# Optimization experiments

Hardware: AMD Instinct MI355X
Metric: run time of the kernel (lower is better)

## Reference

```python
import jax, jax.numpy as jnp
import numpy as np

N = 100000      # nodes
E = 1600000     # edges (before self-loops)
F_IN = 128      # num_features
H = 4           # heads
C = 32          # out_channels per head (num_hidden)
SLOPE = 0.2     # leaky relu negative slope (alpha)


def setup_inputs() -> dict:
    key = jax.random.key(0)
    k = jax.random.split(key, 6)
    x = jax.random.normal(k[0], (N, F_IN), jnp.float32)
    edge_index = jax.random.randint(k[1], (2, E), 0, N, dtype=jnp.int64)
    W = jax.random.normal(k[2], (F_IN, H * C), jnp.float32) * (1.0 / np.sqrt(F_IN))
    att_src = jax.random.normal(k[3], (H, C), jnp.float32) * 0.1
    att_dst = jax.random.normal(k[4], (H, C), jnp.float32) * 0.1
    bias = jnp.zeros((H * C,), jnp.float32)
    return dict(x=x, W=W, att_src=att_src, att_dst=att_dst, bias=bias,
                edge_index=edge_index)


def reference(x, W, att_src, att_dst, bias, edge_index):
    # PyG GATConv (concat=True, add_self_loops=True), eval mode (dropout off).
    loops = jnp.arange(N, dtype=edge_index.dtype)
    ei = jnp.concatenate([edge_index, jnp.stack([loops, loops])], axis=1)
    src, dst = ei[0], ei[1]                     # [E+N]

    h = (x @ W).reshape(N, H, C)                # projected node features
    a_src = jnp.einsum('nhc,hc->nh', h, att_src)   # [N, H]
    a_dst = jnp.einsum('nhc,hc->nh', h, att_dst)   # [N, H]

    e = a_src[src] + a_dst[dst]                 # [E+N, H]
    e = jnp.where(e > 0, e, SLOPE * e)          # leaky relu

    # segment softmax over incoming edges of each dst node (per head)
    m = jax.lax.stop_gradient(jax.ops.segment_max(e, dst, num_segments=N))
    p = jnp.exp(e - m[dst])
    denom = jax.ops.segment_sum(p, dst, num_segments=N)
    alpha = p / (denom[dst] + 1e-16)            # [E+N, H]

    # weighted scatter-aggregate of source features
    out = jax.ops.segment_sum(alpha[:, :, None] * h[src], dst, num_segments=N)
    return out.reshape(N, H * C) + bias
```

## Files before the change

### kernel.cpp

```cpp
#include <hip/hip_runtime.h>
#include <hip/hip_bf16.h>
#include <math.h>

#define N_NODES 100000
#define F_IN    128
#define HC      128
#define NH      4
#define SLOPE   0.2f

#define NB      196
#define BSH     9
#define CAP     10240
#define CHUNK   8192
#define PADK    136

typedef __attribute__((ext_vector_type(8))) short short8;
typedef __attribute__((ext_vector_type(4))) float f32x4;
typedef __attribute__((ext_vector_type(2))) float fx2;

static __device__ __forceinline__ float leaky(float x) { return x > 0.f ? x : SLOPE * x; }

static __device__ __forceinline__ short f2bs(float f) {
    __hip_bfloat16 b = __float2bfloat16(f);
    return *reinterpret_cast<short*>(&b);
}

__global__ __launch_bounds__(256) void k_gemm(const float* __restrict__ x,
                                              const float* __restrict__ W,
                                              const float* __restrict__ att_src,
                                              const float* __restrict__ att_dst,
                                              unsigned short* __restrict__ hb,
                                              float* __restrict__ a_src,
                                              float* __restrict__ a_dst)
{
    __shared__ short xs[64 * PADK];
    __shared__ short ws[128 * PADK];
    const int t  = threadIdx.x;
    const int r0 = blockIdx.x * 64;

    for (int i = t; i < 2048; i += 256) {
        int row = i >> 5, kq = (i & 31) * 4;
        int gr = r0 + row;
        float4 v = make_float4(0.f, 0.f, 0.f, 0.f);
        if (gr < N_NODES) v = ((const float4*)(x + (size_t)gr * F_IN))[i & 31];
        short* p = &xs[row * PADK + kq];
        p[0] = f2bs(v.x); p[1] = f2bs(v.y); p[2] = f2bs(v.z); p[3] = f2bs(v.w);
    }
    for (int i = t; i < 4096; i += 256) {
        int k = i >> 5, nq = (i & 31) * 4;
        float4 v = *(const float4*)&W[k * HC + nq];
        ws[(nq + 0) * PADK + k] = f2bs(v.x);
        ws[(nq + 1) * PADK + k] = f2bs(v.y);
        ws[(nq + 2) * PADK + k] = f2bs(v.z);
        ws[(nq + 3) * PADK + k] = f2bs(v.w);
    }
    __syncthreads();

    const int wave = t >> 6, lane = t & 63;
    const int quad = lane >> 4, l16 = lane & 15;
    const int wrow = wave * 16;

    f32x4 acc[8];
    #pragma unroll
    for (int nt = 0; nt < 8; ++nt) acc[nt] = (f32x4){0.f, 0.f, 0.f, 0.f};

    const short* ap = &xs[(wrow + l16) * PADK + quad * 8];
    #pragma unroll
    for (int kb = 0; kb < 4; ++kb) {
        short8 a = *(const short8*)(ap + kb * 32);
        #pragma unroll
        for (int nt = 0; nt < 8; ++nt) {
            short8 b = *(const short8*)&ws[(nt * 16 + l16) * PADK + kb * 32 + quad * 8];
            acc[nt] = __builtin_amdgcn_mfma_f32_16x16x32_bf16(a, b, acc[nt], 0, 0, 0);
        }
    }

    float att_s[8], att_d[8];
    #pragma unroll
    for (int nt = 0; nt < 8; ++nt) {
        att_s[nt] = att_src[nt * 16 + l16];
        att_d[nt] = att_dst[nt * 16 + l16];
    }

    #pragma unroll
    for (int g = 0; g < 4; ++g) {
        int r = r0 + wrow + quad * 4 + g;
        if (r < N_NODES) {
            #pragma unroll
            for (int nt = 0; nt < 8; ++nt)
                hb[(size_t)r * HC + nt * 16 + l16] = (unsigned short)f2bs(acc[nt][g]);
        }
        float s0 = acc[0][g] * att_s[0] + acc[1][g] * att_s[1];
        float s1 = acc[2][g] * att_s[2] + acc[3][g] * att_s[3];
        float s2 = acc[4][g] * att_s[4] + acc[5][g] * att_s[5];
        float s3 = acc[6][g] * att_s[6] + acc[7][g] * att_s[7];
        float d0 = acc[0][g] * att_d[0] + acc[1][g] * att_d[1];
        float d1 = acc[2][g] * att_d[2] + acc[3][g] * att_d[3];
        float d2 = acc[4][g] * att_d[4] + acc[5][g] * att_d[5];
        float d3 = acc[6][g] * att_d[6] + acc[7][g] * att_d[7];
        #pragma unroll
        for (int o = 1; o < 16; o <<= 1) {
            s0 += __shfl_xor(s0, o); s1 += __shfl_xor(s1, o);
            s2 += __shfl_xor(s2, o); s3 += __shfl_xor(s3, o);
            d0 += __shfl_xor(d0, o); d1 += __shfl_xor(d1, o);
            d2 += __shfl_xor(d2, o); d3 += __shfl_xor(d3, o);
        }
        if (l16 == 0 && r < N_NODES) {
            *(float4*)&a_src[r * NH] = make_float4(s0, s1, s2, s3);
            *(float4*)&a_dst[r * NH] = make_float4(d0, d1, d2, d3);
        }
    }
}

__global__ __launch_bounds__(256) void k_bucket(const int* __restrict__ srcp,
                                                const int* __restrict__ dstp,
                                                int* __restrict__ bucket_cursor,
                                                int* __restrict__ eb, int E)
{
    __shared__ int ebuf[CHUNK];
    __shared__ unsigned char bkt[CHUNK];
    __shared__ int hist[256];
    __shared__ int lexcl[257];
    __shared__ int gbase[256];
    __shared__ int sdata[256];

    const int t = threadIdx.x;
    const int base = blockIdx.x * CHUNK;

    hist[t] = 0;
    __syncthreads();

    #pragma unroll
    for (int j = 0; j < CHUNK / 256; ++j) {
        int i = base + t + j * 256;
        if (i < E) atomicAdd(&hist[dstp[i] >> BSH], 1);
    }
    __syncthreads();

    int cnt = hist[t];
    sdata[t] = cnt;
    __syncthreads();
    for (int o = 1; o < 256; o <<= 1) {
        int add = (t >= o) ? sdata[t - o] : 0;
        __syncthreads();
        sdata[t] += add;
        __syncthreads();
    }
    int excl = sdata[t] - cnt;
    lexcl[t] = excl;
    if (t == 255) lexcl[256] = sdata[255];
    hist[t] = excl;
    int gb = 0;
    if (t < NB && cnt > 0) gb = atomicAdd(&bucket_cursor[t], cnt);
    gbase[t] = t * CAP + gb;
    __syncthreads();

    #pragma unroll
    for (int j = 0; j < CHUNK / 256; ++j) {
        int i = base + t + j * 256;
        if (i < E) {
            int s = srcp[i], d = dstp[i];
            int b = d >> BSH;
            int r = atomicAdd(&hist[b], 1);
            ebuf[r] = (s << BSH) | (d & 511);
            bkt[r] = (unsigned char)b;
        }
    }
    __syncthreads();

    const int blockTotal = lexcl[256];
    for (int i = t; i < blockTotal; i += 256) {
        int b = bkt[i];
        eb[gbase[b] + (i - lexcl[b])] = ebuf[i];
    }
}

__global__ void k_bscan(const int* __restrict__ bucket_cursor,
                        int* __restrict__ bexcl)
{
    __shared__ int sdata[256];
    const int t = threadIdx.x;
    int nvalid = 0;
    if (t < NB) {
        int n0 = t * 512;
        nvalid = min(512, N_NODES - n0);
        if (nvalid < 0) nvalid = 0;
    }
    int v = (t < NB) ? bucket_cursor[t] + nvalid : 0;
    sdata[t] = v;
    __syncthreads();
    for (int o = 1; o < 256; o <<= 1) {
        int add = (t >= o) ? sdata[t - o] : 0;
        __syncthreads();
        sdata[t] += add;
        __syncthreads();
    }
    if (t < NB) bexcl[t] = sdata[t] - v;
}

__global__ __launch_bounds__(256) void k_csr(const int* __restrict__ eb,
                                             const int* __restrict__ bucket_cursor,
                                             const int* __restrict__ bexcl,
                                             int* __restrict__ col,
                                             int2* __restrict__ rowse)
{
    __shared__ int deg[512];
    __shared__ int sdata[256];

    const int t  = threadIdx.x;
    const int b  = blockIdx.x;
    const int n0 = b * 512;
    const int cnt   = bucket_cursor[b];
    const int ebase = b * CAP;
    const int gofs  = bexcl[b];

    deg[t]       = (n0 + t       < N_NODES) ? 1 : 0;
    deg[t + 256] = (n0 + t + 256 < N_NODES) ? 1 : 0;
    __syncthreads();

    for (int i = t; i < cnt; i += 256)
        atomicAdd(&deg[eb[ebase + i] & 511], 1);
    __syncthreads();

    int d0 = deg[2 * t], d1 = deg[2 * t + 1];
    int ps = d0 + d1;
    sdata[t] = ps;
    __syncthreads();
    for (int o = 1; o < 256; o <<= 1) {
        int add = (t >= o) ? sdata[t - o] : 0;
        __syncthreads();
        sdata[t] += add;
        __syncthreads();
    }
    int e0 = sdata[t] - ps;
    int e1 = e0 + d0;
    __syncthreads();

    int na = n0 + 2 * t, nb2 = n0 + 2 * t + 1;
    if (na < N_NODES) {
        rowse[na] = make_int2(gofs + e0, gofs + e0 + d0);
        col[gofs + e0] = na;
    }
    if (nb2 < N_NODES) {
        rowse[nb2] = make_int2(gofs + e1, gofs + e1 + d1);
        col[gofs + e1] = nb2;
    }
    deg[2 * t]     = e0 + 1;
    deg[2 * t + 1] = e1 + 1;
    __syncthreads();

    for (int i = t; i < cnt; i += 256) {
        int v = eb[ebase + i];
        int r = atomicAdd(&deg[v & 511], 1);
        col[gofs + r] = v >> BSH;
    }
}

__global__ __launch_bounds__(256) void k_node(const unsigned short* __restrict__ hb,
                                              const float* __restrict__ a_src,
                                              const float* __restrict__ a_dst,
                                              const int2* __restrict__ rowse,
                                              const int* __restrict__ col,
                                              const float* __restrict__ bias,
                                              float* __restrict__ out)
{
    const int lane = threadIdx.x & 63;
    const int node = blockIdx.x * 4 + (threadIdx.x >> 6);
    if (node >= N_NODES) return;

    const int2 se = rowse[node];
    const int r0 = se.x, r1 = se.y;
    const int myh = lane >> 4;
    const float adm = a_dst[node * NH + myh];

    float denom = 0.f, acc0 = 0.f, acc1 = 0.f;
    int i = r0;
    for (; i + 8 <= r1; i += 8) {
        int s[8];
        #pragma unroll
        for (int j = 0; j < 8; ++j) s[j] = col[i + j];
        float as[8];
        #pragma unroll
        for (int j = 0; j < 8; ++j) as[j] = a_src[s[j] * NH + myh];
        unsigned int hv[8];
        #pragma unroll
        for (int j = 0; j < 8; ++j)
            hv[j] = *(const unsigned int*)&hb[(size_t)s[j] * HC + 2 * lane];
        #pragma unroll
        for (int j = 0; j < 8; ++j) {
            float p = __expf(leaky(as[j] + adm));
            denom += p;
            acc0 += p * __uint_as_float(hv[j] << 16);
            acc1 += p * __uint_as_float(hv[j] & 0xffff0000u);
        }
    }
    for (; i < r1; ++i) {
        int s = col[i];
        float p = __expf(leaky(a_src[s * NH + myh] + adm));
        unsigned int v = *(const unsigned int*)&hb[(size_t)s * HC + 2 * lane];
        denom += p;
        acc0 += p * __uint_as_float(v << 16);
        acc1 += p * __uint_as_float(v & 0xffff0000u);
    }

    float inv = 1.f / (denom + 1e-16f);
    fx2 o2;
    o2.x = acc0 * inv + bias[2 * lane];
    o2.y = acc1 * inv + bias[2 * lane + 1];
    __builtin_nontemporal_store(o2, (fx2*)&out[(size_t)node * HC + 2 * lane]);
}

extern "C" void kernel_launch(void* const* d_in, const int* in_sizes, int n_in,
                              void* d_out, int out_size, void* d_ws, size_t ws_size,
                              hipStream_t stream)
{
    const float* x       = (const float*)d_in[0];
    const float* W       = (const float*)d_in[1];
    const float* att_src = (const float*)d_in[2];
    const float* att_dst = (const float*)d_in[3];
    const float* bias    = (const float*)d_in[4];
    const int*   ei      = (const int*)d_in[5];
    const int E = in_sizes[5] / 2;
    const int* srcp = ei;
    const int* dstp = ei + E;
    float* out = (float*)d_out;

    char* wsb = (char*)d_ws;
    size_t off = 0;
    auto alloc = [&](size_t bytes) -> char* {
        char* p = wsb + off;
        off += (bytes + 255) & ~(size_t)255;
        return p;
    };
    unsigned short* hb = (unsigned short*)alloc((size_t)N_NODES * HC * sizeof(unsigned short));
    float* a_src   = (float*)alloc((size_t)N_NODES * NH * sizeof(float));
    float* a_dst   = (float*)alloc((size_t)N_NODES * NH * sizeof(float));
    int*   eb      = (int*)alloc((size_t)NB * CAP * sizeof(int));
    int*   col     = (int*)alloc((size_t)(E + N_NODES) * sizeof(int));
    int2*  rowse   = (int2*)alloc((size_t)N_NODES * sizeof(int2));
    int*   bcursor = (int*)alloc(256 * sizeof(int));
    int*   bexcl   = (int*)alloc(256 * sizeof(int));

    (void)hipMemsetAsync(bcursor, 0, 256 * sizeof(int), stream);

    k_gemm<<<(N_NODES + 63) / 64, 256, 0, stream>>>(x, W, att_src, att_dst,
                                                    hb, a_src, a_dst);
    k_bucket<<<(E + CHUNK - 1) / CHUNK, 256, 0, stream>>>(srcp, dstp, bcursor, eb, E);
    k_bscan<<<1, 256, 0, stream>>>(bcursor, bexcl);
    k_csr<<<NB, 256, 0, stream>>>(eb, bcursor, bexcl, col, rowse);
    k_node<<<(N_NODES + 3) / 4, 256, 0, stream>>>(hb, a_src, a_dst, rowse, col, bias, out);
}
```

Baseline: 291.6 us.

## Pre-transpose W once, pad bucket cursors, shrink bucket chunks, widen CSR blocks

Adds a small prep kernel that converts W to bf16 and transposes it once, so each GEMM block copies it with vector loads instead of redoing the strided conversion. Bucket cursors are padded so per-bucket atomics land on separate cache lines. The bucket chunk size drops, giving more blocks for the scatter phase. The CSR build runs 1024 threads per block to use more of the GPU across its 196 blocks. These trade an extra launch and more global atomics for better parallelism and less redundant work.

New measurement: 265.8 us. -8.8%, faster.

```diff
diff --git a/kernel.cpp b/kernel.cpp
--- a/kernel.cpp
+++ b/kernel.cpp
@@ -8,11 +8,13 @@
 #define NH      4
 #define SLOPE   0.2f
 
+#define PADK    136
+
 #define NB      196
 #define BSH     9
 #define CAP     10240
-#define CHUNK   8192
-#define PADK    136
+#define CHUNK   2048
+#define CURPAD  16
 
 typedef __attribute__((ext_vector_type(8))) short short8;
 typedef __attribute__((ext_vector_type(4))) float f32x4;
@@ -25,8 +27,18 @@
     return *reinterpret_cast<short*>(&b);
 }
 
+__global__ __launch_bounds__(256) void k_prep(const float* __restrict__ W,
+                                              unsigned short* __restrict__ wt)
+{
+    int t = blockIdx.x * 256 + threadIdx.x;
+    if (t < 128 * 128) {
+        int k = t >> 7, n = t & 127;
+        wt[n * 128 + k] = (unsigned short)f2bs(W[k * HC + n]);
+    }
+}
+
 __global__ __launch_bounds__(256) void k_gemm(const float* __restrict__ x,
-                                              const float* __restrict__ W,
+                                              const unsigned short* __restrict__ wt,
                                               const float* __restrict__ att_src,
                                               const float* __restrict__ att_dst,
                                               unsigned short* __restrict__ hb,
@@ -46,13 +58,9 @@
         short* p = &xs[row * PADK + kq];
         p[0] = f2bs(v.x); p[1] = f2bs(v.y); p[2] = f2bs(v.z); p[3] = f2bs(v.w);
     }
-    for (int i = t; i < 4096; i += 256) {
-        int k = i >> 5, nq = (i & 31) * 4;
-        float4 v = *(const float4*)&W[k * HC + nq];
-        ws[(nq + 0) * PADK + k] = f2bs(v.x);
-        ws[(nq + 1) * PADK + k] = f2bs(v.y);
-        ws[(nq + 2) * PADK + k] = f2bs(v.z);
-        ws[(nq + 3) * PADK + k] = f2bs(v.w);
+    for (int i = t; i < 2048; i += 256) {
+        int n = i >> 4, k0 = (i & 15) * 8;
+        *(float4*)&ws[n * PADK + k0] = *(const float4*)&wt[n * 128 + k0];
     }
     __syncthreads();
 
@@ -151,7 +159,7 @@
     if (t == 255) lexcl[256] = sdata[255];
     hist[t] = excl;
     int gb = 0;
-    if (t < NB && cnt > 0) gb = atomicAdd(&bucket_cursor[t], cnt);
+    if (t < NB && cnt > 0) gb = atomicAdd(&bucket_cursor[t * CURPAD], cnt);
     gbase[t] = t * CAP + gb;
     __syncthreads();
 
@@ -186,7 +194,7 @@
         nvalid = min(512, N_NODES - n0);
         if (nvalid < 0) nvalid = 0;
     }
-    int v = (t < NB) ? bucket_cursor[t] + nvalid : 0;
+    int v = (t < NB) ? bucket_cursor[t * CURPAD] + nvalid : 0;
     sdata[t] = v;
     __syncthreads();
     for (int o = 1; o < 256; o <<= 1) {
@@ -198,11 +206,11 @@
     if (t < NB) bexcl[t] = sdata[t] - v;
 }
 
-__global__ __launch_bounds__(256) void k_csr(const int* __restrict__ eb,
-                                             const int* __restrict__ bucket_cursor,
-                                             const int* __restrict__ bexcl,
-                                             int* __restrict__ col,
-                                             int2* __restrict__ rowse)
+__global__ __launch_bounds__(1024) void k_csr(const int* __restrict__ eb,
+                                              const int* __restrict__ bucket_cursor,
+                                              const int* __restrict__ bexcl,
+                                              int* __restrict__ col,
+                                              int2* __restrict__ rowse)
 {
     __shared__ int deg[512];
     __shared__ int sdata[256];
@@ -210,46 +218,49 @@
     const int t  = threadIdx.x;
     const int b  = blockIdx.x;
     const int n0 = b * 512;
-    const int cnt   = bucket_cursor[b];
+    const int cnt   = bucket_cursor[b * CURPAD];
     const int ebase = b * CAP;
     const int gofs  = bexcl[b];
 
-    deg[t]       = (n0 + t       < N_NODES) ? 1 : 0;
-    deg[t + 256] = (n0 + t + 256 < N_NODES) ? 1 : 0;
-    __syncthreads();
-
-    for (int i = t; i < cnt; i += 256)
+    if (t < 512) deg[t] = (n0 + t < N_NODES) ? 1 : 0;
+    __syncthreads();
+
+    for (int i = t; i < cnt; i += 1024)
         atomicAdd(&deg[eb[ebase + i] & 511], 1);
     __syncthreads();
 
-    int d0 = deg[2 * t], d1 = deg[2 * t + 1];
-    int ps = d0 + d1;
-    sdata[t] = ps;
+    int d0 = 0, d1 = 0, ps = 0;
+    if (t < 256) {
+        d0 = deg[2 * t]; d1 = deg[2 * t + 1];
+        ps = d0 + d1;
+        sdata[t] = ps;
+    }
     __syncthreads();
     for (int o = 1; o < 256; o <<= 1) {
-        int add = (t >= o) ? sdata[t - o] : 0;
-        __syncthreads();
-        sdata[t] += add;
-        __syncthreads();
-    }
-    int e0 = sdata[t] - ps;
-    int e1 = e0 + d0;
-    __syncthreads();
-
-    int na = n0 + 2 * t, nb2 = n0 + 2 * t + 1;
-    if (na < N_NODES) {
-        rowse[na] = make_int2(gofs + e0, gofs + e0 + d0);
-        col[gofs + e0] = na;
-    }
-    if (nb2 < N_NODES) {
-        rowse[nb2] = make_int2(gofs + e1, gofs + e1 + d1);
-        col[gofs + e1] = nb2;
-    }
-    deg[2 * t]     = e0 + 1;
-    deg[2 * t + 1] = e1 + 1;
-    __syncthreads();
-
-    for (int i = t; i < cnt; i += 256) {
+        int add = 0;
+        if (t < 256 && t >= o) add = sdata[t - o];
+        __syncthreads();
+        if (t < 256) sdata[t] += add;
+        __syncthreads();
+    }
+    if (t < 256) {
+        int e0 = sdata[t] - ps;
+        int e1 = e0 + d0;
+        int na = n0 + 2 * t, nb2 = n0 + 2 * t + 1;
+        if (na < N_NODES) {
+            rowse[na] = make_int2(gofs + e0, gofs + e0 + d0);
+            col[gofs + e0] = na;
+        }
+        if (nb2 < N_NODES) {
+            rowse[nb2] = make_int2(gofs + e1, gofs + e1 + d1);
+            col[gofs + e1] = nb2;
+        }
+        deg[2 * t]     = e0 + 1;
+        deg[2 * t + 1] = e1 + 1;
+    }
+    __syncthreads();
+
+    for (int i = t; i < cnt; i += 1024) {
         int v = eb[ebase + i];
         int r = atomicAdd(&deg[v & 511], 1);
         col[gofs + r] = v >> BSH;
@@ -338,15 +349,17 @@
     int*   eb      = (int*)alloc((size_t)NB * CAP * sizeof(int));
     int*   col     = (int*)alloc((size_t)(E + N_NODES) * sizeof(int));
     int2*  rowse   = (int2*)alloc((size_t)N_NODES * sizeof(int2));
-    int*   bcursor = (int*)alloc(256 * sizeof(int));
+    int*   bcursor = (int*)alloc((size_t)NB * CURPAD * sizeof(int));
     int*   bexcl   = (int*)alloc(256 * sizeof(int));
-
-    (void)hipMemsetAsync(bcursor, 0, 256 * sizeof(int), stream);
-
-    k_gemm<<<(N_NODES + 63) / 64, 256, 0, stream>>>(x, W, att_src, att_dst,
+    unsigned short* wt = (unsigned short*)alloc(128 * 128 * sizeof(unsigned short));
+
+    (void)hipMemsetAsync(bcursor, 0, (size_t)NB * CURPAD * sizeof(int), stream);
+
+    k_prep<<<64, 256, 0, stream>>>(W, wt);
+    k_gemm<<<(N_NODES + 63) / 64, 256, 0, stream>>>(x, wt, att_src, att_dst,
                                                     hb, a_src, a_dst);
     k_bucket<<<(E + CHUNK - 1) / CHUNK, 256, 0, stream>>>(srcp, dstp, bcursor, eb, E);
     k_bscan<<<1, 256, 0, stream>>>(bcursor, bexcl);
-    k_csr<<<NB, 256, 0, stream>>>(eb, bcursor, bexcl, col, rowse);
+    k_csr<<<NB, 1024, 0, stream>>>(eb, bcursor, bexcl, col, rowse);
     k_node<<<(N_NODES + 3) / 4, 256, 0, stream>>>(hb, a_src, a_dst, rowse, col, bias, out);
 }
```
